# Performance work log

Hardware: AMD Instinct MI355X
Metric: run time of the kernel (lower is better)

Reference implementation:

```python
import jax, jax.numpy as jnp
import numpy as np

T, H, I, E, K = 1024, 2880, 2880, 16, 4
ALPHA = 1.702   # gemm1_alpha
LIMIT = 7.0     # swiglu_limit (gemm1_clamp_limit)


def setup_inputs() -> dict:
    key = jax.random.key(0)
    ks = jax.random.split(key, 9)
    s = 0.02  # init scale to keep activations sane
    return {
        "hidden_states": jax.random.normal(ks[0], (T, H), jnp.float32),
        "router_w": jax.random.normal(ks[1], (E, H), jnp.float32) * s,
        "router_b": jax.random.normal(ks[2], (E,), jnp.float32) * s,
        "w_gate": jax.random.normal(ks[3], (E, H, I), jnp.float32) * s,
        "b_gate": jax.random.normal(ks[4], (E, I), jnp.float32) * s,
        "w_up": jax.random.normal(ks[5], (E, H, I), jnp.float32) * s,
        "b_up": jax.random.normal(ks[6], (E, I), jnp.float32) * s,
        "w_down": jax.random.normal(ks[7], (E, I, H), jnp.float32) * s,
        "b_down": jax.random.normal(ks[8], (E, H), jnp.float32) * s,
    }


def reference(hidden_states, router_w, router_b, w_gate, b_gate, w_up, b_up, w_down, b_down):
    x = hidden_states  # [T, H]
    # Router: ReplicatedLinear(hidden_size, num_experts, bias=True)
    logits = x @ router_w.T + router_b            # [T, E]
    # TopK(top_k=K, renormalize=True): softmax -> top-k -> renormalize
    probs = jax.nn.softmax(logits, axis=-1)
    top_w, top_i = jax.lax.top_k(probs, K)        # [T, K]
    top_w = top_w / jnp.sum(top_w, axis=-1, keepdims=True)
    # combine weights scattered back to [T, E] (rows sum to 1)
    comb = jnp.sum(jax.nn.one_hot(top_i, E, dtype=x.dtype) * top_w[..., None], axis=1)
    # Expert grouped GEMM (dense over experts; combine weights zero out unused)
    g = jnp.einsum('th,ehi->eti', x, w_gate) + b_gate[:, None, :]   # [E, T, I]
    u = jnp.einsum('th,ehi->eti', x, w_up) + b_up[:, None, :]       # [E, T, I]
    # gpt-oss clamped swiglu: gate clamp max, up clamp both sides
    g = jnp.minimum(g, LIMIT)
    u = jnp.clip(u, -LIMIT, LIMIT)
    act = (u + 1.0) * (g * jax.nn.sigmoid(g * ALPHA))               # [E, T, I]
    y = jnp.einsum('eti,eih->eth', act, w_down) + b_down[:, None, :]  # [E, T, H]
    out = jnp.einsum('te,eth->th', comb, y)                          # [T, H]
    return out
```

## Files before the change

kernel.cpp:

```cpp
#include <hip/hip_runtime.h>
#include <stdint.h>

#define T_TOK 1024
#define HD 2880
#define ID 2880
#define NE 16
#define NTOP 4

#define BM 128
#define BN 64
#define BK 64
#define NKT (HD / BK)

typedef short bf16x8 __attribute__((ext_vector_type(8)));
typedef float f32x4 __attribute__((ext_vector_type(4)));

__device__ __forceinline__ unsigned short f2bf(float f) {
    union { float f; uint32_t u; } a; a.f = f;
    return (unsigned short)((a.u + 0x7FFFu + ((a.u >> 16) & 1u)) >> 16);
}

__device__ __forceinline__ uint4 pack8(const float* v) {
    union { unsigned short s[8]; uint4 q; } p;
#pragma unroll
    for (int j = 0; j < 8; j++) p.s[j] = f2bf(v[j]);
    return p.q;
}

__global__ __launch_bounds__(256) void k_init(float* __restrict__ out, int* __restrict__ cnt) {
    int i = blockIdx.x * 256 + threadIdx.x;
    ((float4*)out)[i] = make_float4(0.f, 0.f, 0.f, 0.f);
    if (blockIdx.x == 0 && threadIdx.x < NE) cnt[threadIdx.x] = 0;
}

__global__ __launch_bounds__(256) void k_router(
    const float* __restrict__ x, const float* __restrict__ rw, const float* __restrict__ rb,
    float* __restrict__ topw, int* __restrict__ cnt, int* __restrict__ list)
{
    const int t = blockIdx.x;
    const int tid = threadIdx.x;
    float acc[NE];
#pragma unroll
    for (int e = 0; e < NE; e++) acc[e] = 0.f;
    for (int c = tid; c < HD; c += 256) {
        float xv = x[(size_t)t * HD + c];
#pragma unroll
        for (int e = 0; e < NE; e++) acc[e] += xv * rw[(size_t)e * HD + c];
    }
    __shared__ float red[4][NE];
    const int lane = tid & 63, wv = tid >> 6;
#pragma unroll
    for (int e = 0; e < NE; e++) {
        float v = acc[e];
#pragma unroll
        for (int off = 32; off > 0; off >>= 1) v += __shfl_down(v, off, 64);
        if (lane == 0) red[wv][e] = v;
    }
    __syncthreads();
    if (tid == 0) {
        float p[NE];
        float mx = -1e30f;
        for (int e = 0; e < NE; e++) {
            float v = red[0][e] + red[1][e] + red[2][e] + red[3][e] + rb[e];
            p[e] = v; mx = fmaxf(mx, v);
        }
        for (int e = 0; e < NE; e++) p[e] = expf(p[e] - mx);
        int sel[NTOP]; float pw[NTOP]; float ssum = 0.f;
        for (int k = 0; k < NTOP; k++) {
            float best = -1.f; int bi = 0;
            for (int e = 0; e < NE; e++)
                if (p[e] > best) { best = p[e]; bi = e; }
            sel[k] = bi; pw[k] = best; ssum += best; p[bi] = -2.f;
        }
        for (int k = 0; k < NTOP; k++) {
            topw[t * NTOP + k] = pw[k] / ssum;
            int e = sel[k];
            int pos = atomicAdd(&cnt[e], 1);
            list[e * T_TOK + pos] = t * NTOP + k;
        }
    }
}

__global__ void k_scan(const int* __restrict__ cnt, int* __restrict__ offs) {
    if (threadIdx.x == 0 && blockIdx.x == 0) {
        int s = 0;
        for (int e = 0; e < NE; e++) { offs[e] = s; s += cnt[e]; }
        offs[NE] = s;
    }
}

__global__ __launch_bounds__(512) void k_gemm1(
    const float* __restrict__ x,
    const float* __restrict__ wg, const float* __restrict__ bg,
    const float* __restrict__ wu, const float* __restrict__ bu,
    const int* __restrict__ cnt, const int* __restrict__ offs,
    const int* __restrict__ list,
    unsigned short* __restrict__ act)
{
    const int e = blockIdx.z;
    const int count = cnt[e];
    const int m0 = blockIdx.y * BM;
    if (m0 >= count) return;
    const int mcount = min(BM, count - m0);
    const int i0 = blockIdx.x * BN;
    const int tid = threadIdx.x;

    __shared__ uint4 sAq[BM * BK * 2 / 16];
    __shared__ uint4 sGq[BN * BK * 2 / 16];
    __shared__ uint4 sUq[BN * BK * 2 / 16];
    __shared__ int lidx[BM];
    char* sA = (char*)sAq; char* sG = (char*)sGq; char* sU = (char*)sUq;

    if (tid < BM) lidx[tid] = list[e * T_TOK + m0 + min(tid, mcount - 1)];
    __syncthreads();

    const int ar = tid >> 2, acg = tid & 3;
    const int tok = lidx[ar] >> 2;
    const float* asrc = x + (size_t)tok * HD + acg * 16;

    const int wtid = tid & 255;
    const int wc = wtid & 63, whg = wtid >> 6;
    const float* wbase = (tid < 256 ? wg : wu) + ((size_t)e * HD + whg * 16) * ID + i0 + wc;
    char* wdst = (tid < 256 ? sG : sU);

    const int lane = tid & 63, wid = tid >> 6;
    const int wm = wid >> 1, wn = wid & 1;
    const int lr = lane & 15, lk = lane >> 4;

    f32x4 accG[2][2], accU[2][2];
#pragma unroll
    for (int mb = 0; mb < 2; mb++)
#pragma unroll
        for (int cb = 0; cb < 2; cb++) {
            accG[mb][cb] = (f32x4){0.f, 0.f, 0.f, 0.f};
            accU[mb][cb] = (f32x4){0.f, 0.f, 0.f, 0.f};
        }

    for (int kt = 0; kt < NKT; kt++) {
        const int h0 = kt * BK;
        {
            const float* s = asrc + h0;
            float v[16];
#pragma unroll
            for (int p = 0; p < 4; p++) {
                float4 f = ((const float4*)s)[p];
                v[p * 4 + 0] = f.x; v[p * 4 + 1] = f.y; v[p * 4 + 2] = f.z; v[p * 4 + 3] = f.w;
            }
            *(uint4*)(sA + ar * 128 + (((acg * 2) ^ (ar & 7)) * 16)) = pack8(v);
            *(uint4*)(sA + ar * 128 + (((acg * 2 + 1) ^ (ar & 7)) * 16)) = pack8(v + 8);
        }
        {
            const float* s = wbase + (size_t)h0 * ID;
            float v[16];
#pragma unroll
            for (int j = 0; j < 16; j++) v[j] = s[(size_t)j * ID];
            *(uint4*)(wdst + wc * 128 + (((whg * 2) ^ (wc & 7)) * 16)) = pack8(v);
            *(uint4*)(wdst + wc * 128 + (((whg * 2 + 1) ^ (wc & 7)) * 16)) = pack8(v + 8);
        }
        __syncthreads();
#pragma unroll
        for (int ks = 0; ks < 2; ks++) {
            const int s = ks * 4 + lk;
            bf16x8 af[2], gf[2], uf[2];
#pragma unroll
            for (int mb = 0; mb < 2; mb++) {
                int rr = wm * 32 + mb * 16 + lr;
                af[mb] = *(const bf16x8*)(sA + rr * 128 + ((s ^ (rr & 7)) * 16));
            }
#pragma unroll
            for (int cb = 0; cb < 2; cb++) {
                int ii = wn * 32 + cb * 16 + lr;
                gf[cb] = *(const bf16x8*)(sG + ii * 128 + ((s ^ (ii & 7)) * 16));
                uf[cb] = *(const bf16x8*)(sU + ii * 128 + ((s ^ (ii & 7)) * 16));
            }
#pragma unroll
            for (int mb = 0; mb < 2; mb++)
#pragma unroll
                for (int cb = 0; cb < 2; cb++) {
                    accG[mb][cb] = __builtin_amdgcn_mfma_f32_16x16x32_bf16(af[mb], gf[cb], accG[mb][cb], 0, 0, 0);
                    accU[mb][cb] = __builtin_amdgcn_mfma_f32_16x16x32_bf16(af[mb], uf[cb], accU[mb][cb], 0, 0, 0);
                }
        }
        __syncthreads();
    }

    const int gbase = offs[e] + m0;
#pragma unroll
    for (int mb = 0; mb < 2; mb++)
#pragma unroll
        for (int cb = 0; cb < 2; cb++) {
            const int col = i0 + wn * 32 + cb * 16 + lr;
            const float bgv = bg[e * ID + col];
            const float buv = bu[e * ID + col];
#pragma unroll
            for (int q = 0; q < 4; q++) {
                const int r = wm * 32 + mb * 16 + lk * 4 + q;
                if (r < mcount) {
                    float gv = fminf(accG[mb][cb][q] + bgv, 7.0f);
                    float uv = fminf(fmaxf(accU[mb][cb][q] + buv, -7.0f), 7.0f);
                    float av = (uv + 1.0f) * (gv / (1.0f + __expf(-1.702f * gv)));
                    act[(size_t)(gbase + r) * ID + col] = f2bf(av);
                }
            }
        }
}

__global__ __launch_bounds__(512) void k_gemm2(
    const unsigned short* __restrict__ act,
    const float* __restrict__ wd, const float* __restrict__ bd,
    const float* __restrict__ topw,
    const int* __restrict__ cnt, const int* __restrict__ offs,
    const int* __restrict__ list,
    float* __restrict__ out)
{
    const int e = blockIdx.z;
    const int count = cnt[e];
    const int m0 = blockIdx.y * BM;
    if (m0 >= count) return;
    const int mcount = min(BM, count - m0);
    const int h0 = blockIdx.x * BN;
    const int tid = threadIdx.x;
    const int gbase = offs[e] + m0;

    __shared__ uint4 sAq[BM * BK * 2 / 16];
    __shared__ uint4 sWq[BN * BK * 2 / 16];
    __shared__ int lidx[BM];
    char* sA = (char*)sAq; char* sW = (char*)sWq;

    if (tid < BM) lidx[tid] = list[e * T_TOK + m0 + min(tid, mcount - 1)];
    __syncthreads();

    const int ar = tid >> 2, acg = tid & 3;
    const int arow = gbase + min(ar, mcount - 1);
    const unsigned short* asrc = act + (size_t)arow * ID + acg * 16;

    const int wc = tid & 63, whg = tid >> 6;
    const float* wbase = wd + (size_t)e * ID * HD + (size_t)(whg * 8) * HD + h0 + wc;

    const int lane = tid & 63, wid = tid >> 6;
    const int wm = wid >> 1, wn = wid & 1;
    const int lr = lane & 15, lk = lane >> 4;

    f32x4 acc[2][2];
#pragma unroll
    for (int mb = 0; mb < 2; mb++)
#pragma unroll
        for (int cb = 0; cb < 2; cb++) acc[mb][cb] = (f32x4){0.f, 0.f, 0.f, 0.f};

    for (int kt = 0; kt < NKT; kt++) {
        const int k0 = kt * BK;
        {
            const uint4* s = (const uint4*)(asrc + k0);
            *(uint4*)(sA + ar * 128 + (((acg * 2) ^ (ar & 7)) * 16)) = s[0];
            *(uint4*)(sA + ar * 128 + (((acg * 2 + 1) ^ (ar & 7)) * 16)) = s[1];
        }
        {
            const float* s = wbase + (size_t)k0 * HD;
            float v[8];
#pragma unroll
            for (int j = 0; j < 8; j++) v[j] = s[(size_t)j * HD];
            *(uint4*)(sW + wc * 128 + ((whg ^ (wc & 7)) * 16)) = pack8(v);
        }
        __syncthreads();
#pragma unroll
        for (int ks = 0; ks < 2; ks++) {
            const int s = ks * 4 + lk;
            bf16x8 af[2], wf[2];
#pragma unroll
            for (int mb = 0; mb < 2; mb++) {
                int rr = wm * 32 + mb * 16 + lr;
                af[mb] = *(const bf16x8*)(sA + rr * 128 + ((s ^ (rr & 7)) * 16));
            }
#pragma unroll
            for (int cb = 0; cb < 2; cb++) {
                int ii = wn * 32 + cb * 16 + lr;
                wf[cb] = *(const bf16x8*)(sW + ii * 128 + ((s ^ (ii & 7)) * 16));
            }
#pragma unroll
            for (int mb = 0; mb < 2; mb++)
#pragma unroll
                for (int cb = 0; cb < 2; cb++)
                    acc[mb][cb] = __builtin_amdgcn_mfma_f32_16x16x32_bf16(af[mb], wf[cb], acc[mb][cb], 0, 0, 0);
        }
        __syncthreads();
    }

#pragma unroll
    for (int mb = 0; mb < 2; mb++)
#pragma unroll
        for (int cb = 0; cb < 2; cb++) {
            const int col = h0 + wn * 32 + cb * 16 + lr;
            const float bdv = bd[e * HD + col];
#pragma unroll
            for (int q = 0; q < 4; q++) {
                const int r = wm * 32 + mb * 16 + lk * 4 + q;
                if (r < mcount) {
                    int idx = lidx[r];
                    float w = topw[idx];
                    atomicAdd(&out[(size_t)(idx >> 2) * HD + col], w * (acc[mb][cb][q] + bdv));
                }
            }
        }
}

extern "C" void kernel_launch(void* const* d_in, const int* in_sizes, int n_in,
                              void* d_out, int out_size, void* d_ws, size_t ws_size,
                              hipStream_t stream)
{
    const float* x  = (const float*)d_in[0];
    const float* rw = (const float*)d_in[1];
    const float* rb = (const float*)d_in[2];
    const float* wg = (const float*)d_in[3];
    const float* bg = (const float*)d_in[4];
    const float* wu = (const float*)d_in[5];
    const float* bu = (const float*)d_in[6];
    const float* wd = (const float*)d_in[7];
    const float* bd = (const float*)d_in[8];
    float* out = (float*)d_out;

    char* ws = (char*)d_ws;
    int*   cnt  = (int*)(ws + 0);
    int*   offs = (int*)(ws + 256);
    float* topw = (float*)(ws + 1024);
    int*   list = (int*)(ws + 32768);
    unsigned short* act = (unsigned short*)(ws + 131072);

    hipLaunchKernelGGL(k_init, dim3(T_TOK * HD / 1024), dim3(256), 0, stream, out, cnt);
    hipLaunchKernelGGL(k_router, dim3(T_TOK), dim3(256), 0, stream, x, rw, rb, topw, cnt, list);
    hipLaunchKernelGGL(k_scan, dim3(1), dim3(64), 0, stream, cnt, offs);
    hipLaunchKernelGGL(k_gemm1, dim3(ID / BN, T_TOK / BM, NE), dim3(512), 0, stream,
                       x, wg, bg, wu, bu, cnt, offs, list, act);
    hipLaunchKernelGGL(k_gemm2, dim3(HD / BN, T_TOK / BM, NE), dim3(512), 0, stream,
                       act, wd, bd, topw, cnt, offs, list, out);
}
```

Baseline: 896.3 us.

## Double-buffer LDS with register prefetch and XCD-aware block remap in both GEMMs

Both expert GEMMs now prefetch the next K tile from global memory into registers while the MFMAs run on the current LDS buffer. The prefetched tile is then written into a second LDS buffer, so each iteration needs one barrier instead of two. The 3D grid is flattened to 1D and remapped so that consecutive logical blocks (the m-blocks of one expert and column tile) land on the same XCD, which is meant to improve L2 reuse of weights. The manual bf16 rounding is replaced with the native __bf16 conversion. The cost is doubled LDS use and more live registers, which could lower occupancy.

```diff
diff --git a/kernel.cpp b/kernel.cpp
--- a/kernel.cpp
+++ b/kernel.cpp
@@ -11,20 +11,23 @@
 #define BN 64
 #define BK 64
 #define NKT (HD / BK)
+#define NIB (ID / BN)
+#define NMB (T_TOK / BM)
+#define NB1 (NE * NIB * NMB)
 
 typedef short bf16x8 __attribute__((ext_vector_type(8)));
 typedef float f32x4 __attribute__((ext_vector_type(4)));
 
-__device__ __forceinline__ unsigned short f2bf(float f) {
-    union { float f; uint32_t u; } a; a.f = f;
-    return (unsigned short)((a.u + 0x7FFFu + ((a.u >> 16) & 1u)) >> 16);
-}
-
-__device__ __forceinline__ uint4 pack8(const float* v) {
-    union { unsigned short s[8]; uint4 q; } p;
-#pragma unroll
-    for (int j = 0; j < 8; j++) p.s[j] = f2bf(v[j]);
+__device__ __forceinline__ uint4 pack8f(const float* v) {
+    union { __bf16 b[8]; uint4 q; } p;
+#pragma unroll
+    for (int j = 0; j < 8; j++) p.b[j] = (__bf16)v[j];
     return p.q;
+}
+__device__ __forceinline__ unsigned short bf16bits(float f) {
+    union { __bf16 b[2]; unsigned short u[2]; } p;
+    p.b[0] = (__bf16)f;
+    return p.u[0];
 }
 
 __global__ __launch_bounds__(256) void k_init(float* __restrict__ out, int* __restrict__ cnt) {
@@ -97,36 +100,66 @@
     const int* __restrict__ list,
     unsigned short* __restrict__ act)
 {
-    const int e = blockIdx.z;
+    const int lin = blockIdx.x;
+    const int logical = (lin & 7) * (NB1 / 8) + (lin >> 3);
+    const int mblk = logical & 7;
+    const int iblk = (logical >> 3) % NIB;
+    const int e = logical / (NIB * NMB);
+
     const int count = cnt[e];
-    const int m0 = blockIdx.y * BM;
+    const int m0 = mblk * BM;
     if (m0 >= count) return;
     const int mcount = min(BM, count - m0);
-    const int i0 = blockIdx.x * BN;
+    const int i0 = iblk * BN;
     const int tid = threadIdx.x;
 
-    __shared__ uint4 sAq[BM * BK * 2 / 16];
-    __shared__ uint4 sGq[BN * BK * 2 / 16];
-    __shared__ uint4 sUq[BN * BK * 2 / 16];
+    __shared__ char sA[2][BM * BK * 2];
+    __shared__ char sG[2][BN * BK * 2];
+    __shared__ char sU[2][BN * BK * 2];
     __shared__ int lidx[BM];
-    char* sA = (char*)sAq; char* sG = (char*)sGq; char* sU = (char*)sUq;
 
     if (tid < BM) lidx[tid] = list[e * T_TOK + m0 + min(tid, mcount - 1)];
     __syncthreads();
 
     const int ar = tid >> 2, acg = tid & 3;
-    const int tok = lidx[ar] >> 2;
-    const float* asrc = x + (size_t)tok * HD + acg * 16;
+    const float* asrc = x + (size_t)(lidx[ar] >> 2) * HD + acg * 16;
 
     const int wtid = tid & 255;
     const int wc = wtid & 63, whg = wtid >> 6;
-    const float* wbase = (tid < 256 ? wg : wu) + ((size_t)e * HD + whg * 16) * ID + i0 + wc;
-    char* wdst = (tid < 256 ? sG : sU);
+    const float* wsrc = (tid < 256 ? wg : wu) + ((size_t)e * HD + whg * 16) * ID + i0 + wc;
+    char* const wdst0 = (tid < 256 ? sG[0] : sU[0]);
+    char* const wdst1 = (tid < 256 ? sG[1] : sU[1]);
 
     const int lane = tid & 63, wid = tid >> 6;
     const int wm = wid >> 1, wn = wid & 1;
     const int lr = lane & 15, lk = lane >> 4;
 
+    float4 ra[4];
+    float rwv[16];
+
+#define LOAD1(kt) do { \
+        const float* s_ = asrc + (kt) * BK; \
+        ra[0] = ((const float4*)s_)[0]; ra[1] = ((const float4*)s_)[1]; \
+        ra[2] = ((const float4*)s_)[2]; ra[3] = ((const float4*)s_)[3]; \
+        const float* w_ = wsrc + (size_t)(kt) * BK * ID; \
+        _Pragma("unroll") \
+        for (int j_ = 0; j_ < 16; j_++) rwv[j_] = w_[(size_t)j_ * ID]; \
+    } while (0)
+
+#define STORE1(buf) do { \
+        float v_[16]; \
+        _Pragma("unroll") \
+        for (int p_ = 0; p_ < 4; p_++) { \
+            v_[p_ * 4 + 0] = ra[p_].x; v_[p_ * 4 + 1] = ra[p_].y; \
+            v_[p_ * 4 + 2] = ra[p_].z; v_[p_ * 4 + 3] = ra[p_].w; \
+        } \
+        *(uint4*)(sA[buf] + ar * 128 + (((acg * 2) ^ (ar & 7)) * 16)) = pack8f(v_); \
+        *(uint4*)(sA[buf] + ar * 128 + (((acg * 2 + 1) ^ (ar & 7)) * 16)) = pack8f(v_ + 8); \
+        char* wd_ = (buf) ? wdst1 : wdst0; \
+        *(uint4*)(wd_ + wc * 128 + (((whg * 2) ^ (wc & 7)) * 16)) = pack8f(rwv); \
+        *(uint4*)(wd_ + wc * 128 + (((whg * 2 + 1) ^ (wc & 7)) * 16)) = pack8f(rwv + 8); \
+    } while (0)
+
     f32x4 accG[2][2], accU[2][2];
 #pragma unroll
     for (int mb = 0; mb < 2; mb++)
@@ -136,28 +169,17 @@
             accU[mb][cb] = (f32x4){0.f, 0.f, 0.f, 0.f};
         }
 
+    LOAD1(0);
+    STORE1(0);
+    __syncthreads();
+
     for (int kt = 0; kt < NKT; kt++) {
-        const int h0 = kt * BK;
-        {
-            const float* s = asrc + h0;
-            float v[16];
-#pragma unroll
-            for (int p = 0; p < 4; p++) {
-                float4 f = ((const float4*)s)[p];
-                v[p * 4 + 0] = f.x; v[p * 4 + 1] = f.y; v[p * 4 + 2] = f.z; v[p * 4 + 3] = f.w;
-            }
-            *(uint4*)(sA + ar * 128 + (((acg * 2) ^ (ar & 7)) * 16)) = pack8(v);
-            *(uint4*)(sA + ar * 128 + (((acg * 2 + 1) ^ (ar & 7)) * 16)) = pack8(v + 8);
-        }
-        {
-            const float* s = wbase + (size_t)h0 * ID;
-            float v[16];
-#pragma unroll
-            for (int j = 0; j < 16; j++) v[j] = s[(size_t)j * ID];
-            *(uint4*)(wdst + wc * 128 + (((whg * 2) ^ (wc & 7)) * 16)) = pack8(v);
-            *(uint4*)(wdst + wc * 128 + (((whg * 2 + 1) ^ (wc & 7)) * 16)) = pack8(v + 8);
-        }
-        __syncthreads();
+        const int cur = kt & 1;
+        const bool more = (kt + 1 < NKT);
+        if (more) LOAD1(kt + 1);
+        const char* cA = sA[cur];
+        const char* cG = sG[cur];
+        const char* cU = sU[cur];
 #pragma unroll
         for (int ks = 0; ks < 2; ks++) {
             const int s = ks * 4 + lk;
@@ -165,13 +187,13 @@
 #pragma unroll
             for (int mb = 0; mb < 2; mb++) {
                 int rr = wm * 32 + mb * 16 + lr;
-                af[mb] = *(const bf16x8*)(sA + rr * 128 + ((s ^ (rr & 7)) * 16));
+                af[mb] = *(const bf16x8*)(cA + rr * 128 + ((s ^ (rr & 7)) * 16));
             }
 #pragma unroll
             for (int cb = 0; cb < 2; cb++) {
                 int ii = wn * 32 + cb * 16 + lr;
-                gf[cb] = *(const bf16x8*)(sG + ii * 128 + ((s ^ (ii & 7)) * 16));
-                uf[cb] = *(const bf16x8*)(sU + ii * 128 + ((s ^ (ii & 7)) * 16));
+                gf[cb] = *(const bf16x8*)(cG + ii * 128 + ((s ^ (ii & 7)) * 16));
+                uf[cb] = *(const bf16x8*)(cU + ii * 128 + ((s ^ (ii & 7)) * 16));
             }
 #pragma unroll
             for (int mb = 0; mb < 2; mb++)
@@ -181,8 +203,11 @@
                     accU[mb][cb] = __builtin_amdgcn_mfma_f32_16x16x32_bf16(af[mb], uf[cb], accU[mb][cb], 0, 0, 0);
                 }
         }
+        if (more) STORE1(cur ^ 1);
         __syncthreads();
     }
+#undef LOAD1
+#undef STORE1
 
     const int gbase = offs[e] + m0;
 #pragma unroll
@@ -199,7 +224,7 @@
                     float gv = fminf(accG[mb][cb][q] + bgv, 7.0f);
                     float uv = fminf(fmaxf(accU[mb][cb][q] + buv, -7.0f), 7.0f);
                     float av = (uv + 1.0f) * (gv / (1.0f + __expf(-1.702f * gv)));
-                    act[(size_t)(gbase + r) * ID + col] = f2bf(av);
+                    act[(size_t)(gbase + r) * ID + col] = bf16bits(av);
                 }
             }
         }
@@ -213,19 +238,23 @@
     const int* __restrict__ list,
     float* __restrict__ out)
 {
-    const int e = blockIdx.z;
+    const int lin = blockIdx.x;
+    const int logical = (lin & 7) * (NB1 / 8) + (lin >> 3);
+    const int mblk = logical & 7;
+    const int hblk = (logical >> 3) % NIB;
+    const int e = logical / (NIB * NMB);
+
     const int count = cnt[e];
-    const int m0 = blockIdx.y * BM;
+    const int m0 = mblk * BM;
     if (m0 >= count) return;
     const int mcount = min(BM, count - m0);
-    const int h0 = blockIdx.x * BN;
+    const int h0 = hblk * BN;
     const int tid = threadIdx.x;
     const int gbase = offs[e] + m0;
 
-    __shared__ uint4 sAq[BM * BK * 2 / 16];
-    __shared__ uint4 sWq[BN * BK * 2 / 16];
+    __shared__ char sA[2][BM * BK * 2];
+    __shared__ char sW[2][BN * BK * 2];
     __shared__ int lidx[BM];
-    char* sA = (char*)sAq; char* sW = (char*)sWq;
 
     if (tid < BM) lidx[tid] = list[e * T_TOK + m0 + min(tid, mcount - 1)];
     __syncthreads();
@@ -235,33 +264,45 @@
     const unsigned short* asrc = act + (size_t)arow * ID + acg * 16;
 
     const int wc = tid & 63, whg = tid >> 6;
-    const float* wbase = wd + (size_t)e * ID * HD + (size_t)(whg * 8) * HD + h0 + wc;
+    const float* wsrc = wd + (size_t)e * ID * HD + (size_t)(whg * 8) * HD + h0 + wc;
 
     const int lane = tid & 63, wid = tid >> 6;
     const int wm = wid >> 1, wn = wid & 1;
     const int lr = lane & 15, lk = lane >> 4;
 
+    uint4 ra0, ra1;
+    float rwv[8];
+
+#define LOAD2(kt) do { \
+        const uint4* s_ = (const uint4*)(asrc + (kt) * BK); \
+        ra0 = s_[0]; ra1 = s_[1]; \
+        const float* w_ = wsrc + (size_t)(kt) * BK * HD; \
+        _Pragma("unroll") \
+        for (int j_ = 0; j_ < 8; j_++) rwv[j_] = w_[(size_t)j_ * HD]; \
+    } while (0)
+
+#define STORE2(buf) do { \
+        *(uint4*)(sA[buf] + ar * 128 + (((acg * 2) ^ (ar & 7)) * 16)) = ra0; \
+        *(uint4*)(sA[buf] + ar * 128 + (((acg * 2 + 1) ^ (ar & 7)) * 16)) = ra1; \
+        *(uint4*)(sW[buf] + wc * 128 + ((whg ^ (wc & 7)) * 16)) = pack8f(rwv); \
+    } while (0)
+
     f32x4 acc[2][2];
 #pragma unroll
     for (int mb = 0; mb < 2; mb++)
 #pragma unroll
         for (int cb = 0; cb < 2; cb++) acc[mb][cb] = (f32x4){0.f, 0.f, 0.f, 0.f};
 
+    LOAD2(0);
+    STORE2(0);
+    __syncthreads();
+
     for (int kt = 0; kt < NKT; kt++) {
-        const int k0 = kt * BK;
-        {
-            const uint4* s = (const uint4*)(asrc + k0);
-            *(uint4*)(sA + ar * 128 + (((acg * 2) ^ (ar & 7)) * 16)) = s[0];
-            *(uint4*)(sA + ar * 128 + (((acg * 2 + 1) ^ (ar & 7)) * 16)) = s[1];
-        }
-        {
-            const float* s = wbase + (size_t)k0 * HD;
-            float v[8];
-#pragma unroll
-            for (int j = 0; j < 8; j++) v[j] = s[(size_t)j * HD];
-            *(uint4*)(sW + wc * 128 + ((whg ^ (wc & 7)) * 16)) = pack8(v);
-        }
-        __syncthreads();
+        const int cur = kt & 1;
+        const bool more = (kt + 1 < NKT);
+        if (more) LOAD2(kt + 1);
+        const char* cA = sA[cur];
+        const char* cW = sW[cur];
 #pragma unroll
         for (int ks = 0; ks < 2; ks++) {
             const int s = ks * 4 + lk;
@@ -269,12 +310,12 @@
 #pragma unroll
             for (int mb = 0; mb < 2; mb++) {
                 int rr = wm * 32 + mb * 16 + lr;
-                af[mb] = *(const bf16x8*)(sA + rr * 128 + ((s ^ (rr & 7)) * 16));
+                af[mb] = *(const bf16x8*)(cA + rr * 128 + ((s ^ (rr & 7)) * 16));
             }
 #pragma unroll
             for (int cb = 0; cb < 2; cb++) {
                 int ii = wn * 32 + cb * 16 + lr;
-                wf[cb] = *(const bf16x8*)(sW + ii * 128 + ((s ^ (ii & 7)) * 16));
+                wf[cb] = *(const bf16x8*)(cW + ii * 128 + ((s ^ (ii & 7)) * 16));
             }
 #pragma unroll
             for (int mb = 0; mb < 2; mb++)
@@ -282,8 +323,11 @@
                 for (int cb = 0; cb < 2; cb++)
                     acc[mb][cb] = __builtin_amdgcn_mfma_f32_16x16x32_bf16(af[mb], wf[cb], acc[mb][cb], 0, 0, 0);
         }
+        if (more) STORE2(cur ^ 1);
         __syncthreads();
     }
+#undef LOAD2
+#undef STORE2
 
 #pragma unroll
     for (int mb = 0; mb < 2; mb++)
@@ -328,8 +372,8 @@
     hipLaunchKernelGGL(k_init, dim3(T_TOK * HD / 1024), dim3(256), 0, stream, out, cnt);
     hipLaunchKernelGGL(k_router, dim3(T_TOK), dim3(256), 0, stream, x, rw, rb, topw, cnt, list);
     hipLaunchKernelGGL(k_scan, dim3(1), dim3(64), 0, stream, cnt, offs);
-    hipLaunchKernelGGL(k_gemm1, dim3(ID / BN, T_TOK / BM, NE), dim3(512), 0, stream,
+    hipLaunchKernelGGL(k_gemm1, dim3(NB1), dim3(512), 0, stream,
                        x, wg, bg, wu, bu, cnt, offs, list, act);
-    hipLaunchKernelGGL(k_gemm2, dim3(HD / BN, T_TOK / BM, NE), dim3(512), 0, stream,
+    hipLaunchKernelGGL(k_gemm2, dim3(NB1), dim3(512), 0, stream,
                        act, wd, bd, topw, cnt, offs, list, out);
 }
```

New measurement: 1.082 ms. 20.7% more time.

## Pre-convert x to bf16, load A tiles via global_load_lds, remap blocks across XCDs

Applied to the files above, without the earlier changes.

Adds a kernel that converts hidden states to bf16 once, so the gather of A-tile rows no longer converts fp32 to bf16 inside every GEMM1 block. Both GEMMs now fill their A tiles with direct global-to-LDS loads, keeping the existing XOR swizzle through the per-lane source offset. Launches become a flat 1D grid whose block index is permuted so neighbouring logical tiles (same expert and column block) land on the same XCD, which should improve L2 reuse of weight tiles. It also switches to the compiler's native bf16 conversion and costs an extra kernel launch plus a bf16 copy of x.

```diff
diff --git a/kernel.cpp b/kernel.cpp
--- a/kernel.cpp
+++ b/kernel.cpp
@@ -11,26 +11,39 @@
 #define BN 64
 #define BK 64
 #define NKT (HD / BK)
+#define NIB (ID / BN)
+#define NMB (T_TOK / BM)
+#define NBLK (NE * NIB * NMB)
 
 typedef short bf16x8 __attribute__((ext_vector_type(8)));
 typedef float f32x4 __attribute__((ext_vector_type(4)));
 
-__device__ __forceinline__ unsigned short f2bf(float f) {
-    union { float f; uint32_t u; } a; a.f = f;
-    return (unsigned short)((a.u + 0x7FFFu + ((a.u >> 16) & 1u)) >> 16);
-}
-
-__device__ __forceinline__ uint4 pack8(const float* v) {
-    union { unsigned short s[8]; uint4 q; } p;
-#pragma unroll
-    for (int j = 0; j < 8; j++) p.s[j] = f2bf(v[j]);
+__device__ __forceinline__ uint4 pack8f(const float* v) {
+    union { __bf16 b[8]; uint4 q; } p;
+#pragma unroll
+    for (int j = 0; j < 8; j++) p.b[j] = (__bf16)v[j];
     return p.q;
+}
+__device__ __forceinline__ unsigned short bf16bits(float f) {
+    union { __bf16 b[2]; unsigned short u[2]; } p;
+    p.b[0] = (__bf16)f;
+    return p.u[0];
 }
 
 __global__ __launch_bounds__(256) void k_init(float* __restrict__ out, int* __restrict__ cnt) {
     int i = blockIdx.x * 256 + threadIdx.x;
     ((float4*)out)[i] = make_float4(0.f, 0.f, 0.f, 0.f);
     if (blockIdx.x == 0 && threadIdx.x < NE) cnt[threadIdx.x] = 0;
+}
+
+__global__ __launch_bounds__(256) void k_xbf(const float* __restrict__ x, unsigned short* __restrict__ xbf) {
+    const size_t i = (size_t)blockIdx.x * 256 + threadIdx.x;
+    float v[8];
+    float4 a = ((const float4*)x)[i * 2];
+    float4 b = ((const float4*)x)[i * 2 + 1];
+    v[0] = a.x; v[1] = a.y; v[2] = a.z; v[3] = a.w;
+    v[4] = b.x; v[5] = b.y; v[6] = b.z; v[7] = b.w;
+    ((uint4*)xbf)[i] = pack8f(v);
 }
 
 __global__ __launch_bounds__(256) void k_router(
@@ -90,43 +103,51 @@
 }
 
 __global__ __launch_bounds__(512) void k_gemm1(
-    const float* __restrict__ x,
+    const unsigned short* __restrict__ xbf,
     const float* __restrict__ wg, const float* __restrict__ bg,
     const float* __restrict__ wu, const float* __restrict__ bu,
     const int* __restrict__ cnt, const int* __restrict__ offs,
     const int* __restrict__ list,
     unsigned short* __restrict__ act)
 {
-    const int e = blockIdx.z;
+    const int lin = blockIdx.x;
+    const int logical = (lin & 7) * (NBLK / 8) + (lin >> 3);
+    const int mblk = logical & 7;
+    const int iblk = (logical >> 3) % NIB;
+    const int e = logical / (NIB * NMB);
+
     const int count = cnt[e];
-    const int m0 = blockIdx.y * BM;
+    const int m0 = mblk * BM;
     if (m0 >= count) return;
     const int mcount = min(BM, count - m0);
-    const int i0 = blockIdx.x * BN;
+    const int i0 = iblk * BN;
     const int tid = threadIdx.x;
 
-    __shared__ uint4 sAq[BM * BK * 2 / 16];
-    __shared__ uint4 sGq[BN * BK * 2 / 16];
-    __shared__ uint4 sUq[BN * BK * 2 / 16];
+    __shared__ char sA[BM * BK * 2];
+    __shared__ char sG[BN * BK * 2];
+    __shared__ char sU[BN * BK * 2];
     __shared__ int lidx[BM];
-    char* sA = (char*)sAq; char* sG = (char*)sGq; char* sU = (char*)sUq;
 
     if (tid < BM) lidx[tid] = list[e * T_TOK + m0 + min(tid, mcount - 1)];
     __syncthreads();
-
-    const int ar = tid >> 2, acg = tid & 3;
-    const int tok = lidx[ar] >> 2;
-    const float* asrc = x + (size_t)tok * HD + acg * 16;
-
-    const int wtid = tid & 255;
-    const int wc = wtid & 63, whg = wtid >> 6;
-    const float* wbase = (tid < 256 ? wg : wu) + ((size_t)e * HD + whg * 16) * ID + i0 + wc;
-    char* wdst = (tid < 256 ? sG : sU);
 
     const int lane = tid & 63, wid = tid >> 6;
     const int wm = wid >> 1, wn = wid & 1;
     const int lr = lane & 15, lk = lane >> 4;
 
+    const int arw0 = wid * 8 + (lane >> 3);
+    const int arw1 = 64 + arw0;
+    const int asl = ((lane & 7) ^ ((lane >> 3) & 7)) * 8;
+    const unsigned short* ga0 = xbf + (size_t)(lidx[arw0] >> 2) * HD + asl;
+    const unsigned short* ga1 = xbf + (size_t)(lidx[arw1] >> 2) * HD + asl;
+    char* const lb0 = sA + (wid * 8) * 128;
+    char* const lb1 = sA + (64 + wid * 8) * 128;
+
+    const int wtid = tid & 255;
+    const int wc = wtid & 63, whg = wtid >> 6;
+    const float* wsrc = (tid < 256 ? wg : wu) + ((size_t)e * HD + whg * 16) * ID + i0 + wc;
+    char* const wdst = (tid < 256 ? sG : sU);
+
     f32x4 accG[2][2], accU[2][2];
 #pragma unroll
     for (int mb = 0; mb < 2; mb++)
@@ -137,25 +158,14 @@
         }
 
     for (int kt = 0; kt < NKT; kt++) {
-        const int h0 = kt * BK;
+        __builtin_amdgcn_global_load_lds(ga0 + kt * BK, lb0, 16, 0, 0);
+        __builtin_amdgcn_global_load_lds(ga1 + kt * BK, lb1, 16, 0, 0);
         {
-            const float* s = asrc + h0;
             float v[16];
 #pragma unroll
-            for (int p = 0; p < 4; p++) {
-                float4 f = ((const float4*)s)[p];
-                v[p * 4 + 0] = f.x; v[p * 4 + 1] = f.y; v[p * 4 + 2] = f.z; v[p * 4 + 3] = f.w;
-            }
-            *(uint4*)(sA + ar * 128 + (((acg * 2) ^ (ar & 7)) * 16)) = pack8(v);
-            *(uint4*)(sA + ar * 128 + (((acg * 2 + 1) ^ (ar & 7)) * 16)) = pack8(v + 8);
-        }
-        {
-            const float* s = wbase + (size_t)h0 * ID;
-            float v[16];
-#pragma unroll
-            for (int j = 0; j < 16; j++) v[j] = s[(size_t)j * ID];
-            *(uint4*)(wdst + wc * 128 + (((whg * 2) ^ (wc & 7)) * 16)) = pack8(v);
-            *(uint4*)(wdst + wc * 128 + (((whg * 2 + 1) ^ (wc & 7)) * 16)) = pack8(v + 8);
+            for (int j = 0; j < 16; j++) v[j] = wsrc[(size_t)(kt * BK + j) * ID];
+            *(uint4*)(wdst + wc * 128 + (((whg * 2) ^ (wc & 7)) * 16)) = pack8f(v);
+            *(uint4*)(wdst + wc * 128 + (((whg * 2 + 1) ^ (wc & 7)) * 16)) = pack8f(v + 8);
         }
         __syncthreads();
 #pragma unroll
@@ -199,7 +209,7 @@
                     float gv = fminf(accG[mb][cb][q] + bgv, 7.0f);
                     float uv = fminf(fmaxf(accU[mb][cb][q] + buv, -7.0f), 7.0f);
                     float av = (uv + 1.0f) * (gv / (1.0f + __expf(-1.702f * gv)));
-                    act[(size_t)(gbase + r) * ID + col] = f2bf(av);
+                    act[(size_t)(gbase + r) * ID + col] = bf16bits(av);
                 }
             }
         }
@@ -213,34 +223,42 @@
     const int* __restrict__ list,
     float* __restrict__ out)
 {
-    const int e = blockIdx.z;
+    const int lin = blockIdx.x;
+    const int logical = (lin & 7) * (NBLK / 8) + (lin >> 3);
+    const int mblk = logical & 7;
+    const int hblk = (logical >> 3) % NIB;
+    const int e = logical / (NIB * NMB);
+
     const int count = cnt[e];
-    const int m0 = blockIdx.y * BM;
+    const int m0 = mblk * BM;
     if (m0 >= count) return;
     const int mcount = min(BM, count - m0);
-    const int h0 = blockIdx.x * BN;
+    const int h0 = hblk * BN;
     const int tid = threadIdx.x;
     const int gbase = offs[e] + m0;
 
-    __shared__ uint4 sAq[BM * BK * 2 / 16];
-    __shared__ uint4 sWq[BN * BK * 2 / 16];
+    __shared__ char sA[BM * BK * 2];
+    __shared__ char sW[BN * BK * 2];
     __shared__ int lidx[BM];
-    char* sA = (char*)sAq; char* sW = (char*)sWq;
 
     if (tid < BM) lidx[tid] = list[e * T_TOK + m0 + min(tid, mcount - 1)];
     __syncthreads();
-
-    const int ar = tid >> 2, acg = tid & 3;
-    const int arow = gbase + min(ar, mcount - 1);
-    const unsigned short* asrc = act + (size_t)arow * ID + acg * 16;
-
-    const int wc = tid & 63, whg = tid >> 6;
-    const float* wbase = wd + (size_t)e * ID * HD + (size_t)(whg * 8) * HD + h0 + wc;
 
     const int lane = tid & 63, wid = tid >> 6;
     const int wm = wid >> 1, wn = wid & 1;
     const int lr = lane & 15, lk = lane >> 4;
 
+    const int arw0 = wid * 8 + (lane >> 3);
+    const int arw1 = 64 + arw0;
+    const int asl = ((lane & 7) ^ ((lane >> 3) & 7)) * 8;
+    const unsigned short* ga0 = act + (size_t)(gbase + min(arw0, mcount - 1)) * ID + asl;
+    const unsigned short* ga1 = act + (size_t)(gbase + min(arw1, mcount - 1)) * ID + asl;
+    char* const lb0 = sA + (wid * 8) * 128;
+    char* const lb1 = sA + (64 + wid * 8) * 128;
+
+    const int wc = tid & 63, whg = tid >> 6;
+    const float* wsrc = wd + (size_t)e * ID * HD + (size_t)(whg * 8) * HD + h0 + wc;
+
     f32x4 acc[2][2];
 #pragma unroll
     for (int mb = 0; mb < 2; mb++)
@@ -248,18 +266,13 @@
         for (int cb = 0; cb < 2; cb++) acc[mb][cb] = (f32x4){0.f, 0.f, 0.f, 0.f};
 
     for (int kt = 0; kt < NKT; kt++) {
-        const int k0 = kt * BK;
+        __builtin_amdgcn_global_load_lds(ga0 + kt * BK, lb0, 16, 0, 0);
+        __builtin_amdgcn_global_load_lds(ga1 + kt * BK, lb1, 16, 0, 0);
         {
-            const uint4* s = (const uint4*)(asrc + k0);
-            *(uint4*)(sA + ar * 128 + (((acg * 2) ^ (ar & 7)) * 16)) = s[0];
-            *(uint4*)(sA + ar * 128 + (((acg * 2 + 1) ^ (ar & 7)) * 16)) = s[1];
-        }
-        {
-            const float* s = wbase + (size_t)k0 * HD;
             float v[8];
 #pragma unroll
-            for (int j = 0; j < 8; j++) v[j] = s[(size_t)j * HD];
-            *(uint4*)(sW + wc * 128 + ((whg ^ (wc & 7)) * 16)) = pack8(v);
+            for (int j = 0; j < 8; j++) v[j] = wsrc[(size_t)(kt * BK + j) * HD];
+            *(uint4*)(sW + wc * 128 + ((whg ^ (wc & 7)) * 16)) = pack8f(v);
         }
         __syncthreads();
 #pragma unroll
@@ -324,12 +337,14 @@
     float* topw = (float*)(ws + 1024);
     int*   list = (int*)(ws + 32768);
     unsigned short* act = (unsigned short*)(ws + 131072);
+    unsigned short* xbf = (unsigned short*)(ws + 131072 + (size_t)4096 * ID * 2);
 
     hipLaunchKernelGGL(k_init, dim3(T_TOK * HD / 1024), dim3(256), 0, stream, out, cnt);
+    hipLaunchKernelGGL(k_xbf, dim3(T_TOK * HD / (256 * 8)), dim3(256), 0, stream, x, xbf);
     hipLaunchKernelGGL(k_router, dim3(T_TOK), dim3(256), 0, stream, x, rw, rb, topw, cnt, list);
     hipLaunchKernelGGL(k_scan, dim3(1), dim3(64), 0, stream, cnt, offs);
-    hipLaunchKernelGGL(k_gemm1, dim3(ID / BN, T_TOK / BM, NE), dim3(512), 0, stream,
-                       x, wg, bg, wu, bu, cnt, offs, list, act);
-    hipLaunchKernelGGL(k_gemm2, dim3(HD / BN, T_TOK / BM, NE), dim3(512), 0, stream,
+    hipLaunchKernelGGL(k_gemm1, dim3(NBLK), dim3(512), 0, stream,
+                       xbf, wg, bg, wu, bu, cnt, offs, list, act);
+    hipLaunchKernelGGL(k_gemm2, dim3(NBLK), dim3(512), 0, stream,
                        act, wd, bd, topw, cnt, offs, list, out);
 }
```

Result: slower. 1.094 ms (+22.0%).
